# Kernel optimization log

Hardware: AMD Instinct MI355X
Metric: run time of the kernel (lower is better)

Reference implementation:

```python
import jax, jax.numpy as jnp
import numpy as np

# Static hyperparams matching init_kwargs
KSIZE, STRIDE, PAD, DIL = 3, 2, 1, 1


def setup_inputs() -> dict:
    key = jax.random.key(0)
    k1, k2 = jax.random.split(key)
    B, H, W, Cin, Cout = 8, 128, 128, 128, 256
    feats = jax.random.normal(k1, (B * H * W, Cin), dtype=jnp.float32)
    weight = jax.random.normal(k2, (KSIZE * KSIZE, Cin, Cout), dtype=jnp.float32) * 0.05
    alpha_upper = jnp.ones((1,), dtype=jnp.float32)
    # dense grid coords [N, 3] = (batch, y, x), matching a dense image sparse tensor
    bb, yy, xx = np.meshgrid(np.arange(B), np.arange(H), np.arange(W), indexing='ij')
    coords = jnp.asarray(np.stack([bb, yy, xx], -1).reshape(-1, 3), dtype=jnp.int32)
    return {"feats": feats, "weight": weight, "alpha_upper": alpha_upper,
            "coords": coords, "H": H, "W": W, "B": B}


def _coord_ranges(H, W):
    # Faithful translation of WrappedMinkowskiStridedOperation.__init__ + forward
    # coordinate math, specialized to a dense grid (per-batch min=0, max=H-1/W-1).
    kernel_origin = DIL * ((KSIZE - 1) // 2) * (KSIZE % 2)
    dilated = DIL * (KSIZE - 1) + 1
    ks_off = kernel_origin - dilated + 1          # _kernel_start_offset
    ke_off = kernel_origin                        # _kernel_end_offset
    idx_start = kernel_origin - PAD               # _index_start_offset
    ranges = []
    for ext in (H, W):
        idx_end = (ext - 1) + kernel_origin + PAD - dilated + 2
        start = max(idx_start, (0 + ks_off - idx_start) // STRIDE * STRIDE + idx_start)
        end = min(idx_end, ((ext - 1 + ke_off - idx_start) // STRIDE + 1) * STRIDE + idx_start)
        ranges.append(np.arange(start, end, STRIDE))
    offsets = np.arange(KSIZE) * DIL - kernel_origin  # kernel region offsets
    return ranges[0], ranges[1], offsets, idx_start


def reference(feats, weight, alpha_upper, coords, H, W, B):
    Cin = feats.shape[1]
    Cout = weight.shape[-1]
    ys, xs, offs, idx_start = _coord_ranges(H, W)
    OH, OW = len(ys), len(xs)
    oy, ox = jnp.meshgrid(jnp.asarray(ys, jnp.int32), jnp.asarray(xs, jnp.int32), indexing='ij')
    dy, dx = np.meshgrid(offs, offs, indexing='ij')
    dy = jnp.asarray(dy.reshape(-1), jnp.int32)  # [kvol]
    dx = jnp.asarray(dx.reshape(-1), jnp.int32)
    ny = oy[None] + dy[:, None, None]            # [kvol, OH, OW]
    nx = ox[None] + dx[:, None, None]
    valid = (ny >= 0) & (ny < H) & (nx >= 0) & (nx < W)
    lin = jnp.clip(ny, 0, H - 1) * W + jnp.clip(nx, 0, W - 1)  # [kvol, OH, OW]
    feats3 = feats.reshape(B, H * W, Cin)
    gathered = feats3[:, lin]                    # [B, kvol, OH, OW, Cin]
    gathered = jnp.where(valid[None, ..., None], gathered, jnp.zeros((), feats.dtype))
    out = jnp.einsum('bkhwc,kcd->bhwd', gathered, weight)  # [B, OH, OW, Cout]
    out_feats = out.reshape(B * OH * OW, Cout)
    # output coordinates, remapped as in forward (shift by index_start, divide by stride)
    oc = jnp.stack([oy, ox], -1).reshape(-1, 2)  # [OH*OW, 2]
    oc = (oc - jnp.int32(idx_start)) // jnp.int32(STRIDE)
    oc = jnp.tile(oc, (B, 1))
    bcol = jnp.repeat(jnp.arange(B, dtype=jnp.int32), OH * OW)
    out_coords = jnp.concatenate([bcol[:, None], oc], axis=1)
    return out_feats, out_coords, alpha_upper
```

## Files before the change

### kernel.cpp

```cpp
#include <hip/hip_runtime.h>


#define OUT_FEATS_ELEMS (32768 * 256)
#define OUT_COORDS_OFF  OUT_FEATS_ELEMS
#define ALPHA_OFF       (OUT_FEATS_ELEMS + 32768 * 3)

typedef __bf16 v8bf  __attribute__((ext_vector_type(8)));
typedef float  v16f  __attribute__((ext_vector_type(16)));

__device__ __forceinline__ unsigned short f2bf(float f) {
    union { float f; unsigned u; } v; v.f = f;
    return (unsigned short)((v.u + 0x7fffu + ((v.u >> 16) & 1u)) >> 16);
}

#define GLOAD_LDS16(SRC, DST)                                                  \
    __builtin_amdgcn_global_load_lds(                                          \
        (const __attribute__((address_space(1))) void*)(SRC),                  \
        (__attribute__((address_space(3))) void*)(DST), 16, 0, 0)

__global__ void conv_feats_kernel(const float4* __restrict__ f, ushort4* __restrict__ o) {
    int i = blockIdx.x * 256 + threadIdx.x;
    float4 v = f[i];
    ushort4 r;
    r.x = f2bf(v.x); r.y = f2bf(v.y); r.z = f2bf(v.z); r.w = f2bf(v.w);
    o[i] = r;
}

__global__ void wt_coords_kernel(const float* __restrict__ w, unsigned short* __restrict__ Bw,
                                 float* __restrict__ out, const float* __restrict__ alpha) {
    int cid = blockIdx.x * 256 + threadIdx.x;
    if (cid < 32768) {
        int b = cid >> 12, iy = (cid >> 6) & 63, ix = cid & 63;
        float* c = out + OUT_COORDS_OFF + (size_t)cid * 3;
        c[0] = (float)b; c[1] = (float)iy; c[2] = (float)ix;
        if (cid == 0) out[ALPHA_OFF] = alpha[0];
    }
    int ch  = cid & 15;
    int row = (cid >> 4) & 127;
    int t   = cid >> 11;
    int nb  = (t >= 9) ? 1 : 0;
    int tap = t - 9 * nb;
    int cl  = ch ^ (row & 15);
    int n   = (nb << 7) + row;
    int kb  = (tap << 7) + (cl << 3);
    unsigned short r8[8];
#pragma unroll
    for (int j = 0; j < 8; ++j) r8[j] = f2bf(w[(size_t)(kb + j) * 256 + n]);
    *(uint4*)(Bw + (size_t)cid * 8) = *(const uint4*)r8;
}

__global__ void coords_alpha_kernel(float* __restrict__ out, const float* __restrict__ alpha) {
    int i = blockIdx.x * 256 + threadIdx.x;
    int b = i >> 12, iy = (i >> 6) & 63, ix = i & 63;
    float* c = out + OUT_COORDS_OFF + (size_t)i * 3;
    c[0] = (float)b; c[1] = (float)iy; c[2] = (float)ix;
    if (i == 0) out[ALPHA_OFF] = alpha[0];
}

__global__ __launch_bounds__(256, 2) void gemm_conv_kernel(
    const unsigned short* __restrict__ F,
    const unsigned short* __restrict__ Bw,
    float* __restrict__ out)
{
    __shared__ unsigned short At[128 * 128];
    __shared__ unsigned short Bs[128 * 128];

    const int tid  = threadIdx.x;
    const int bid  = blockIdx.x;
    const int my   = bid & 255;
    const int nb   = bid >> 8;
    const int n0   = nb << 7;
    const int m0   = my << 7;
    const int bb   = my >> 5;
    const int iy0  = (my << 1) & 63;

    const int lane = tid & 63, wave = tid >> 6;
    const int wm   = (wave >> 1) << 6;
    const int wn   = (wave & 1) << 6;
    const int l31  = lane & 31;
    const int hh   = lane >> 5;
    const int xorm = lane & 15;

    const int srow4 = lane >> 4;
    const long rowA0 = (long)bb << 14;
    const unsigned short* bimg = Bw + ((size_t)(nb * 9) << 14) + ((size_t)wave << 12) + ((size_t)lane << 3);
    unsigned short* adst0 = At + (wave << 12);
    unsigned short* bdst0 = Bs + (wave << 12);

    v16f acc[2][2];
#pragma unroll
    for (int i = 0; i < 2; i++)
#pragma unroll
        for (int j = 0; j < 2; j++) acc[i][j] = (v16f)(0.0f);

    for (int tap = 0; tap < 9; ++tap) {
        const int dy = tap / 3 - 1;
        const int dx = tap % 3 - 1;

        __syncthreads();
#pragma unroll
        for (int it = 0; it < 8; ++it) {
            const int region = (wave << 3) + it;
            const int row    = (region << 2) + srow4;
            const int iyl = row >> 6, ix = row & 63;
            const int ny  = ((iy0 + iyl) << 1) + dy;
            const int nx  = (ix << 1) + dx;
            const int chp = xorm ^ (row & 15);
            if (((unsigned)ny < 128u) & ((unsigned)nx < 128u)) {
                const unsigned short* asrc =
                    F + ((rowA0 + ((long)ny << 7) + nx) << 7) + (chp << 3);
                GLOAD_LDS16(asrc, adst0 + (it << 9));
            } else {
                uint4 z; z.x = 0u; z.y = 0u; z.z = 0u; z.w = 0u;
                *(uint4*)(At + (region << 9) + (lane << 3)) = z;
            }
            GLOAD_LDS16(bimg + ((size_t)tap << 14) + (it << 9), bdst0 + (it << 9));
        }
        __syncthreads();

#pragma unroll
        for (int seg = 0; seg < 8; ++seg) {
            v8bf a[2], b[2];
            const int c = ((seg << 1) + hh) ^ xorm;
#pragma unroll
            for (int i = 0; i < 2; i++) {
                const int row = wm + (i << 5) + l31;
                a[i] = *(const v8bf*)(At + (row << 7) + (c << 3));
            }
#pragma unroll
            for (int j = 0; j < 2; j++) {
                const int row = wn + (j << 5) + l31;
                b[j] = *(const v8bf*)(Bs + (row << 7) + (c << 3));
            }
#pragma unroll
            for (int i = 0; i < 2; i++)
#pragma unroll
                for (int j = 0; j < 2; j++)
                    acc[i][j] = __builtin_amdgcn_mfma_f32_32x32x16_bf16(a[i], b[j], acc[i][j], 0, 0, 0);
        }
    }

#pragma unroll
    for (int i = 0; i < 2; i++)
#pragma unroll
        for (int j = 0; j < 2; j++) {
            const int gcol = n0 + wn + (j << 5) + l31;
#pragma unroll
            for (int r = 0; r < 16; ++r) {
                const int grow = m0 + wm + (i << 5) + (r & 3) + ((r >> 2) << 3) + (hh << 2);
                out[(size_t)grow * 256 + gcol] = acc[i][j][r];
            }
        }
}

__global__ void naive_conv_kernel(const float* __restrict__ feats,
                                  const float* __restrict__ w,
                                  float* __restrict__ out) {
    int m = blockIdx.x;
    int n = threadIdx.x;
    int bb = m >> 12, iy = (m >> 6) & 63, ix = m & 63;
    float acc = 0.f;
    for (int tap = 0; tap < 9; ++tap) {
        int ny = 2 * iy + tap / 3 - 1;
        int nx = 2 * ix + tap % 3 - 1;
        if ((unsigned)ny < 128u && (unsigned)nx < 128u) {
            const float* fr = feats + ((size_t)((bb << 14) + (ny << 7) + nx) << 7);
            const float* wr = w + tap * 32768 + n;
            for (int c = 0; c < 128; ++c) acc += fr[c] * wr[c * 256];
        }
    }
    out[(size_t)m * 256 + n] = acc;
}

extern "C" void kernel_launch(void* const* d_in, const int* in_sizes, int n_in,
                              void* d_out, int out_size, void* d_ws, size_t ws_size,
                              hipStream_t stream) {
    const float* feats  = (const float*)d_in[0];
    const float* weight = (const float*)d_in[1];
    const float* alpha  = (const float*)d_in[2];
    float* out = (float*)d_out;

    const size_t NEED = (size_t)16777216 * 2 + (size_t)18 * 16384 * 2;
    if (ws_size >= NEED) {
        unsigned short* Fb = (unsigned short*)d_ws;
        unsigned short* Bw = Fb + 16777216;
        conv_feats_kernel<<<16384, 256, 0, stream>>>((const float4*)feats, (ushort4*)Fb);
        wt_coords_kernel<<<144, 256, 0, stream>>>(weight, Bw, out, alpha);
        gemm_conv_kernel<<<512, 256, 0, stream>>>(Fb, Bw, out);
    } else {
        coords_alpha_kernel<<<128, 256, 0, stream>>>(out, alpha);
        naive_conv_kernel<<<32768, 256, 0, stream>>>(feats, weight, out);
    }
}
```

Baseline: 145.1 us.

## Switch conv GEMM from bf16 to fp8 inputs with fp8 MFMA

```diff
diff --git a/kernel.cpp b/kernel.cpp
--- a/kernel.cpp
+++ b/kernel.cpp
@@ -5,12 +5,13 @@
 #define OUT_COORDS_OFF  OUT_FEATS_ELEMS
 #define ALPHA_OFF       (OUT_FEATS_ELEMS + 32768 * 3)
 
-typedef __bf16 v8bf  __attribute__((ext_vector_type(8)));
-typedef float  v16f  __attribute__((ext_vector_type(16)));
-
-__device__ __forceinline__ unsigned short f2bf(float f) {
-    union { float f; unsigned u; } v; v.f = f;
-    return (unsigned short)((v.u + 0x7fffu + ((v.u >> 16) & 1u)) >> 16);
+typedef float v16f __attribute__((ext_vector_type(16)));
+
+__device__ __forceinline__ unsigned pk4fp8(float a, float b, float c, float d) {
+    unsigned u = 0;
+    u = __builtin_amdgcn_cvt_pk_fp8_f32(a, b, u, false);
+    u = __builtin_amdgcn_cvt_pk_fp8_f32(c, d, u, true);
+    return u;
 }
 
 #define GLOAD_LDS16(SRC, DST)                                                  \
@@ -18,15 +19,17 @@
         (const __attribute__((address_space(1))) void*)(SRC),                  \
         (__attribute__((address_space(3))) void*)(DST), 16, 0, 0)
 
-__global__ void conv_feats_kernel(const float4* __restrict__ f, ushort4* __restrict__ o) {
+__global__ void feats8_kernel(const float4* __restrict__ f, uint2* __restrict__ o) {
     int i = blockIdx.x * 256 + threadIdx.x;
-    float4 v = f[i];
-    ushort4 r;
-    r.x = f2bf(v.x); r.y = f2bf(v.y); r.z = f2bf(v.z); r.w = f2bf(v.w);
+    float4 a = f[2 * i];
+    float4 b = f[2 * i + 1];
+    uint2 r;
+    r.x = pk4fp8(a.x, a.y, a.z, a.w);
+    r.y = pk4fp8(b.x, b.y, b.z, b.w);
     o[i] = r;
 }
 
-__global__ void wt_coords_kernel(const float* __restrict__ w, unsigned short* __restrict__ Bw,
+__global__ void wt_coords_kernel(const float* __restrict__ w, unsigned char* __restrict__ Bw,
                                  float* __restrict__ out, const float* __restrict__ alpha) {
     int cid = blockIdx.x * 256 + threadIdx.x;
     if (cid < 32768) {
@@ -35,18 +38,27 @@
         c[0] = (float)b; c[1] = (float)iy; c[2] = (float)ix;
         if (cid == 0) out[ALPHA_OFF] = alpha[0];
     }
-    int ch  = cid & 15;
-    int row = (cid >> 4) & 127;
-    int t   = cid >> 11;
-    int nb  = (t >= 9) ? 1 : 0;
-    int tap = t - 9 * nb;
-    int cl  = ch ^ (row & 15);
-    int n   = (nb << 7) + row;
-    int kb  = (tap << 7) + (cl << 3);
-    unsigned short r8[8];
-#pragma unroll
-    for (int j = 0; j < 8; ++j) r8[j] = f2bf(w[(size_t)(kb + j) * 256 + n]);
-    *(uint4*)(Bw + (size_t)cid * 8) = *(const uint4*)r8;
+    if (cid < 18432) {
+        int ch  = cid & 7;
+        int row = (cid >> 3) & 127;
+        int t   = cid >> 10;
+        int nb  = (t >= 9) ? 1 : 0;
+        int tap = t - 9 * nb;
+        int chp = ch ^ (row & 7);
+        int n   = (nb << 7) + row;
+        int kb  = (tap << 7) + (chp << 4);
+        unsigned u[4];
+#pragma unroll
+        for (int q = 0; q < 4; ++q) {
+            float f0 = w[(size_t)(kb + 4 * q + 0) * 256 + n];
+            float f1 = w[(size_t)(kb + 4 * q + 1) * 256 + n];
+            float f2 = w[(size_t)(kb + 4 * q + 2) * 256 + n];
+            float f3 = w[(size_t)(kb + 4 * q + 3) * 256 + n];
+            u[q] = pk4fp8(f0, f1, f2, f3);
+        }
+        uint4 r; r.x = u[0]; r.y = u[1]; r.z = u[2]; r.w = u[3];
+        *(uint4*)(Bw + (size_t)cid * 16) = r;
+    }
 }
 
 __global__ void coords_alpha_kernel(float* __restrict__ out, const float* __restrict__ alpha) {
@@ -58,12 +70,12 @@
 }
 
 __global__ __launch_bounds__(256, 2) void gemm_conv_kernel(
-    const unsigned short* __restrict__ F,
-    const unsigned short* __restrict__ Bw,
+    const unsigned char* __restrict__ F8,
+    const unsigned char* __restrict__ Bw,
     float* __restrict__ out)
 {
-    __shared__ unsigned short At[128 * 128];
-    __shared__ unsigned short Bs[128 * 128];
+    __shared__ unsigned char At[128 * 128];
+    __shared__ unsigned char Bs[128 * 128];
 
     const int tid  = threadIdx.x;
     const int bid  = blockIdx.x;
@@ -79,13 +91,14 @@
     const int wn   = (wave & 1) << 6;
     const int l31  = lane & 31;
     const int hh   = lane >> 5;
-    const int xorm = lane & 15;
-
-    const int srow4 = lane >> 4;
+    const int xorl = l31 & 7;
+
+    const int srow = lane >> 3;
+    const int chp  = (lane & 7) ^ srow;
     const long rowA0 = (long)bb << 14;
-    const unsigned short* bimg = Bw + ((size_t)(nb * 9) << 14) + ((size_t)wave << 12) + ((size_t)lane << 3);
-    unsigned short* adst0 = At + (wave << 12);
-    unsigned short* bdst0 = Bs + (wave << 12);
+    const unsigned char* bimg = Bw + ((size_t)(nb * 9) << 14) + ((size_t)wave << 12) + ((size_t)lane << 4);
+    unsigned char* adst0 = At + (wave << 12);
+    unsigned char* bdst0 = Bs + (wave << 12);
 
     v16f acc[2][2];
 #pragma unroll
@@ -99,44 +112,39 @@
 
         __syncthreads();
 #pragma unroll
-        for (int it = 0; it < 8; ++it) {
-            const int region = (wave << 3) + it;
-            const int row    = (region << 2) + srow4;
+        for (int it = 0; it < 4; ++it) {
+            const int region = (wave << 2) + it;
+            GLOAD_LDS16(bimg + ((size_t)tap << 14) + (it << 10), bdst0 + (it << 10));
+            const int row = (region << 3) + srow;
             const int iyl = row >> 6, ix = row & 63;
             const int ny  = ((iy0 + iyl) << 1) + dy;
             const int nx  = (ix << 1) + dx;
-            const int chp = xorm ^ (row & 15);
             if (((unsigned)ny < 128u) & ((unsigned)nx < 128u)) {
-                const unsigned short* asrc =
-                    F + ((rowA0 + ((long)ny << 7) + nx) << 7) + (chp << 3);
-                GLOAD_LDS16(asrc, adst0 + (it << 9));
+                const unsigned char* asrc =
+                    F8 + ((rowA0 + ((long)ny << 7) + nx) << 7) + (chp << 4);
+                GLOAD_LDS16(asrc, adst0 + (it << 10));
             } else {
                 uint4 z; z.x = 0u; z.y = 0u; z.z = 0u; z.w = 0u;
-                *(uint4*)(At + (region << 9) + (lane << 3)) = z;
+                *(uint4*)(At + (region << 10) + (lane << 4)) = z;
             }
-            GLOAD_LDS16(bimg + ((size_t)tap << 14) + (it << 9), bdst0 + (it << 9));
         }
         __syncthreads();
 
 #pragma unroll
         for (int seg = 0; seg < 8; ++seg) {
-            v8bf a[2], b[2];
-            const int c = ((seg << 1) + hh) ^ xorm;
-#pragma unroll
-            for (int i = 0; i < 2; i++) {
-                const int row = wm + (i << 5) + l31;
-                a[i] = *(const v8bf*)(At + (row << 7) + (c << 3));
-            }
-#pragma unroll
-            for (int j = 0; j < 2; j++) {
-                const int row = wn + (j << 5) + l31;
-                b[j] = *(const v8bf*)(Bs + (row << 7) + (c << 3));
-            }
+            const int q = seg ^ xorl;
+            long long a[2], b[2];
 #pragma unroll
             for (int i = 0; i < 2; i++)
+                a[i] = *(const long long*)(At + ((wm + (i << 5) + l31) << 7) + (q << 4) + (hh << 3));
+#pragma unroll
+            for (int j = 0; j < 2; j++)
+                b[j] = *(const long long*)(Bs + ((wn + (j << 5) + l31) << 7) + (q << 4) + (hh << 3));
+#pragma unroll
+            for (int i = 0; i < 2; i++)
 #pragma unroll
                 for (int j = 0; j < 2; j++)
-                    acc[i][j] = __builtin_amdgcn_mfma_f32_32x32x16_bf16(a[i], b[j], acc[i][j], 0, 0, 0);
+                    acc[i][j] = __builtin_amdgcn_mfma_f32_32x32x16_fp8_fp8(a[i], b[j], acc[i][j], 0, 0, 0);
         }
     }
 
@@ -180,13 +188,13 @@
     const float* alpha  = (const float*)d_in[2];
     float* out = (float*)d_out;
 
-    const size_t NEED = (size_t)16777216 * 2 + (size_t)18 * 16384 * 2;
+    const size_t NEED = (size_t)16777216 + (size_t)18 * 16384;
     if (ws_size >= NEED) {
-        unsigned short* Fb = (unsigned short*)d_ws;
-        unsigned short* Bw = Fb + 16777216;
-        conv_feats_kernel<<<16384, 256, 0, stream>>>((const float4*)feats, (ushort4*)Fb);
+        unsigned char* F8 = (unsigned char*)d_ws;
+        unsigned char* Bw = F8 + 16777216;
+        feats8_kernel<<<8192, 256, 0, stream>>>((const float4*)feats, (uint2*)F8);
         wt_coords_kernel<<<144, 256, 0, stream>>>(weight, Bw, out, alpha);
-        gemm_conv_kernel<<<512, 256, 0, stream>>>(Fb, Bw, out);
+        gemm_conv_kernel<<<512, 256, 0, stream>>>(F8, Bw, out);
     } else {
         coords_alpha_kernel<<<128, 256, 0, stream>>>(out, alpha);
         naive_conv_kernel<<<32768, 256, 0, stream>>>(feats, weight, out);
```

Result: faster. 136.0 us (-6.2%).
